# Performance work log

Measured on AMD Instinct MI355X. Metric: run time of the kernel, lower is better.

Reference implementation:

```python
import jax, jax.numpy as jnp
import numpy as np

N_NODES = 100000
N_EDGES = 1600000
NFEAT, NHID, NCLASS = 512, 128, 40


def setup_inputs() -> dict:
    key = jax.random.key(0)
    ks = jax.random.split(key, 8)
    x = jax.random.normal(ks[0], (N_NODES, NFEAT), dtype=jnp.float32)
    adj_row = jax.random.randint(ks[1], (N_EDGES,), 0, N_NODES, dtype=jnp.int64)
    adj_col = jax.random.randint(ks[2], (N_EDGES,), 0, N_NODES, dtype=jnp.int64)
    adj_val = jax.random.uniform(ks[3], (N_EDGES,), dtype=jnp.float32)
    W1 = jax.random.normal(ks[4], (NFEAT, NHID), dtype=jnp.float32) * (1.0 / np.sqrt(NHID))
    b1 = jax.random.normal(ks[5], (NHID,), dtype=jnp.float32) * 0.01
    W2 = jax.random.normal(ks[6], (NHID, NCLASS), dtype=jnp.float32) * (1.0 / np.sqrt(NCLASS))
    b2 = jax.random.normal(ks[7], (NCLASS,), dtype=jnp.float32) * 0.01
    return {"x": x, "adj_row": adj_row, "adj_col": adj_col, "adj_val": adj_val,
            "W1": W1, "b1": b1, "W2": W2, "b2": b2}


def _spmm(row, col, val, dense):
    # COO SpMM: out[r] = sum_e val[e] * dense[col[e]]  for edges with row[e]==r
    gathered = val[:, None] * dense[col]          # [E, F]
    return jax.ops.segment_sum(gathered, row, num_segments=N_NODES)


def reference(x, adj_row, adj_col, adj_val, W1, b1, W2, b2):
    # Layer 1: support = X @ W1; out = A @ support + b1; ReLU
    h = _spmm(adj_row, adj_col, adj_val, x @ W1) + b1
    h = jax.nn.relu(h)
    # dropout is identity in eval mode (training=False)
    # Layer 2
    logits = _spmm(adj_row, adj_col, adj_val, h @ W2) + b2
    return jax.nn.log_softmax(logits, axis=1)
```

## Files before the change

kernel.cpp:

```cpp
#include <hip/hip_runtime.h>
#include <hip/hip_bf16.h>
#include <math.h>

#define N_NODES 100000
#define N_EDGES 1600000
#define NFEAT 512
#define NHID 128
#define NCLASS 40
#define CAP 48
#define G1_ROWS 128
#define G1_BLOCKS ((N_NODES + G1_ROWS - 1) / G1_ROWS)
#define COUNT_BLOCKS ((N_EDGES + 1023) / 1024)
#define PITCH 520

typedef __attribute__((ext_vector_type(8))) short short8;
typedef __attribute__((ext_vector_type(4))) float floatx4;

__device__ __forceinline__ short f2bf(float f) {
    union { float f; unsigned u; } v; v.f = f;
    unsigned r = v.u + 0x7FFFu + ((v.u >> 16) & 1u);
    return (short)(r >> 16);
}
__device__ __forceinline__ float bf2f(unsigned short u) {
    union { unsigned u; float f; } v; v.u = ((unsigned)u) << 16;
    return v.f;
}
__device__ __forceinline__ unsigned pk2bf(float a, float b) {
    __hip_bfloat162 t = __float22bfloat162_rn(make_float2(a, b));
    union { __hip_bfloat162 h; unsigned u; } v; v.h = t;
    return v.u;
}

__global__ void convert_W1_kernel(const float* __restrict__ W1, unsigned short* __restrict__ W1T) {
    int i = blockIdx.x * 256 + threadIdx.x;
    int k = i >> 7, n = i & 127;
    W1T[(size_t)n * NFEAT + k] = (unsigned short)f2bf(W1[i]);
}

__global__ __launch_bounds__(512)
void gemm1_kernel(const float* __restrict__ x, const unsigned short* __restrict__ W1T,
                  unsigned short* __restrict__ out) {
    __shared__ unsigned short Bs[NHID * PITCH];
    int t = threadIdx.x;
    {
        const short8* src = (const short8*)W1T;
        #pragma unroll
        for (int i = 0; i < 16; i++) {
            int c = t + i * 512;
            int row = c >> 6;
            int col = (c & 63) * 8;
            *(short8*)&Bs[row * PITCH + col] = src[c];
        }
    }
    __syncthreads();

    int w = t >> 6, l = t & 63;
    int lane16 = l & 15, quad = l >> 4;
    int rowBase = blockIdx.x * G1_ROWS + w * 16;

    floatx4 acc[8];
    #pragma unroll
    for (int j = 0; j < 8; j++) acc[j] = (floatx4){0.f, 0.f, 0.f, 0.f};

    int gr = rowBase + lane16;
    if (gr >= N_NODES) gr = N_NODES - 1;
    const float* aRow = x + (size_t)gr * NFEAT + quad * 8;

    #pragma unroll 4
    for (int kc = 0; kc < NFEAT; kc += 32) {
        float4 v0 = *(const float4*)(aRow + kc);
        float4 v1 = *(const float4*)(aRow + kc + 4);
        union { short8 s; unsigned u[4]; } av;
        av.u[0] = pk2bf(v0.x, v0.y);
        av.u[1] = pk2bf(v0.z, v0.w);
        av.u[2] = pk2bf(v1.x, v1.y);
        av.u[3] = pk2bf(v1.z, v1.w);
        short8 afr = av.s;
        #pragma unroll
        for (int nt = 0; nt < 8; nt++) {
            short8 bfr = *(const short8*)&Bs[(nt * 16 + lane16) * PITCH + kc + quad * 8];
            acc[nt] = __builtin_amdgcn_mfma_f32_16x16x32_bf16(afr, bfr, acc[nt], 0, 0, 0);
        }
    }
    #pragma unroll
    for (int r = 0; r < 4; r++) {
        int gr2 = rowBase + quad * 4 + r;
        if (gr2 < N_NODES) {
            #pragma unroll
            for (int nt = 0; nt < 8; nt++)
                out[(size_t)gr2 * NHID + nt * 16 + lane16] =
                    (unsigned short)f2bf(acc[nt][r]);
        }
    }
}

__global__ __launch_bounds__(256)
void count_fill_kernel(const int* __restrict__ adj_row, const int* __restrict__ adj_col,
                       const float* __restrict__ adj_val,
                       int* __restrict__ counts, int2* __restrict__ csr) {
    int base = blockIdx.x * 1024 + threadIdx.x;
    #pragma unroll
    for (int i = 0; i < 4; i++) {
        int e = base + i * 256;
        if (e < N_EDGES) {
            int r = adj_row[e];
            int old = atomicAdd(&counts[r], 1);
            if (old < CAP)
                csr[(size_t)r * CAP + old] = make_int2(adj_col[e], __float_as_int(adj_val[e]));
        }
    }
}

__global__ __launch_bounds__(256)
void spmm1_kernel(const int* __restrict__ counts, const int2* __restrict__ csr,
                  const unsigned short* __restrict__ dense, const float* __restrict__ b1,
                  unsigned short* __restrict__ h) {
    int r = blockIdx.x * 4 + (threadIdx.x >> 6);
    int l = threadIdx.x & 63;
    int cnt = min(counts[r], CAP);
    int2 pk = (l < cnt) ? csr[(size_t)r * CAP + l] : make_int2(0, 0);
    float acc0 = 0.f, acc1 = 0.f;
    int j = 0;
    for (; j + 16 <= cnt; j += 16) {
        unsigned d[16];
        float v[16];
        #pragma unroll
        for (int q = 0; q < 16; q++) {
            int c = __shfl(pk.x, j + q);
            v[q] = __int_as_float(__shfl(pk.y, j + q));
            d[q] = *(const unsigned*)&dense[(size_t)c * NHID + l * 2];
        }
        #pragma unroll
        for (int q = 0; q < 16; q++) {
            acc0 += v[q] * bf2f((unsigned short)d[q]);
            acc1 += v[q] * bf2f((unsigned short)(d[q] >> 16));
        }
    }
    for (; j + 8 <= cnt; j += 8) {
        unsigned d[8];
        float v[8];
        #pragma unroll
        for (int q = 0; q < 8; q++) {
            int c = __shfl(pk.x, j + q);
            v[q] = __int_as_float(__shfl(pk.y, j + q));
            d[q] = *(const unsigned*)&dense[(size_t)c * NHID + l * 2];
        }
        #pragma unroll
        for (int q = 0; q < 8; q++) {
            acc0 += v[q] * bf2f((unsigned short)d[q]);
            acc1 += v[q] * bf2f((unsigned short)(d[q] >> 16));
        }
    }
    for (; j < cnt; j++) {
        int c = __shfl(pk.x, j);
        float v = __int_as_float(__shfl(pk.y, j));
        unsigned d = *(const unsigned*)&dense[(size_t)c * NHID + l * 2];
        acc0 += v * bf2f((unsigned short)d);
        acc1 += v * bf2f((unsigned short)(d >> 16));
    }
    float r0 = fmaxf(acc0 + b1[l * 2 + 0], 0.f);
    float r1 = fmaxf(acc1 + b1[l * 2 + 1], 0.f);
    *(unsigned*)&h[(size_t)r * NHID + l * 2] = pk2bf(r0, r1);
}

__global__ __launch_bounds__(256)
void gemm2_kernel(const unsigned short* __restrict__ h, const float* __restrict__ W2,
                  unsigned short* __restrict__ out) {
    __shared__ float W2s[NHID * NCLASS];
    __shared__ float hs[32][NHID];
    int t = threadIdx.x;
    for (int i = t; i < NHID * NCLASS; i += 256) W2s[i] = W2[i];
    int row0 = blockIdx.x * 32;
    {
        const unsigned* hsrc = (const unsigned*)(h + (size_t)row0 * NHID);
        #pragma unroll
        for (int j = 0; j < 8; j++) {
            int f = t * 8 + j;
            unsigned d = hsrc[f];
            hs[f >> 6][(f & 63) * 2 + 0] = bf2f((unsigned short)d);
            hs[f >> 6][(f & 63) * 2 + 1] = bf2f((unsigned short)(d >> 16));
        }
    }
    __syncthreads();
    int w = t >> 6, l = t & 63;
    if (l < NCLASS) {
        float acc[8];
        #pragma unroll
        for (int j = 0; j < 8; j++) acc[j] = 0.f;
        #pragma unroll 4
        for (int k = 0; k < NHID; k++) {
            float wk = W2s[k * NCLASS + l];
            #pragma unroll
            for (int j = 0; j < 8; j++) acc[j] += hs[w * 8 + j][k] * wk;
        }
        #pragma unroll
        for (int j = 0; j < 8; j++)
            out[(size_t)(row0 + w * 8 + j) * NCLASS + l] = (unsigned short)f2bf(acc[j]);
    }
}

__global__ __launch_bounds__(256)
void spmm2_kernel(const int* __restrict__ counts, const int2* __restrict__ csr,
                  const unsigned short* __restrict__ dense, const float* __restrict__ b2,
                  float* __restrict__ out) {
    int r = blockIdx.x * 4 + (threadIdx.x >> 6);
    int l = threadIdx.x & 63;
    int cnt = min(counts[r], CAP);
    int2 pk = (l < cnt) ? csr[(size_t)r * CAP + l] : make_int2(0, 0);
    float acc = 0.f;
    int j = 0;
    for (; j + 16 <= cnt; j += 16) {
        float v[16], f[16];
        #pragma unroll
        for (int q = 0; q < 16; q++) {
            int c = __shfl(pk.x, j + q);
            v[q] = __int_as_float(__shfl(pk.y, j + q));
            f[q] = (l < NCLASS) ? bf2f(dense[(size_t)c * NCLASS + l]) : 0.f;
        }
        #pragma unroll
        for (int q = 0; q < 16; q++) acc += v[q] * f[q];
    }
    for (; j + 8 <= cnt; j += 8) {
        float v[8], f[8];
        #pragma unroll
        for (int q = 0; q < 8; q++) {
            int c = __shfl(pk.x, j + q);
            v[q] = __int_as_float(__shfl(pk.y, j + q));
            f[q] = (l < NCLASS) ? bf2f(dense[(size_t)c * NCLASS + l]) : 0.f;
        }
        #pragma unroll
        for (int q = 0; q < 8; q++) acc += v[q] * f[q];
    }
    for (; j < cnt; j++) {
        int c = __shfl(pk.x, j);
        float v = __int_as_float(__shfl(pk.y, j));
        if (l < NCLASS) acc += v * bf2f(dense[(size_t)c * NCLASS + l]);
    }
    float logit = (l < NCLASS) ? (acc + b2[l]) : -INFINITY;
    float m = logit;
    #pragma unroll
    for (int o = 32; o >= 1; o >>= 1) m = fmaxf(m, __shfl_xor(m, o, 64));
    float e = (l < NCLASS) ? __expf(logit - m) : 0.f;
    float s = e;
    #pragma unroll
    for (int o = 32; o >= 1; o >>= 1) s += __shfl_xor(s, o, 64);
    if (l < NCLASS) out[(size_t)r * NCLASS + l] = logit - m - __logf(s);
}


extern "C" void kernel_launch(void* const* d_in, const int* in_sizes, int n_in,
                              void* d_out, int out_size, void* d_ws, size_t ws_size,
                              hipStream_t stream) {
    const float* x       = (const float*)d_in[0];
    const int*   adj_row = (const int*)d_in[1];
    const int*   adj_col = (const int*)d_in[2];
    const float* adj_val = (const float*)d_in[3];
    const float* W1      = (const float*)d_in[4];
    const float* b1      = (const float*)d_in[5];
    const float* W2      = (const float*)d_in[6];
    const float* b2      = (const float*)d_in[7];
    float* out = (float*)d_out;

    char* ws = (char*)d_ws;
    size_t off = 0;
    auto alloc = [&](size_t bytes) -> void* {
        void* p = ws + off;
        off += bytes;
        off = (off + 255) & ~(size_t)255;
        return p;
    };
    unsigned short* support1 = (unsigned short*)alloc((size_t)N_NODES * NHID * 2);
    unsigned short* h        = (unsigned short*)alloc((size_t)N_NODES * NHID * 2);
    unsigned short* W1T      = (unsigned short*)alloc((size_t)NFEAT * NHID * 2);
    int*   counts = (int*)alloc((size_t)N_NODES * 4);
    int2*  csr    = (int2*)alloc((size_t)N_NODES * CAP * 8);
    unsigned short* support2 = support1;

    hipMemsetAsync(counts, 0, (size_t)N_NODES * sizeof(int), stream);
    convert_W1_kernel<<<(NFEAT * NHID) / 256, 256, 0, stream>>>(W1, W1T);
    count_fill_kernel<<<COUNT_BLOCKS, 256, 0, stream>>>(adj_row, adj_col, adj_val,
                                                        counts, csr);
    gemm1_kernel<<<G1_BLOCKS, 512, 0, stream>>>(x, W1T, support1);
    spmm1_kernel<<<N_NODES / 4, 256, 0, stream>>>(counts, csr, support1, b1, h);
    gemm2_kernel<<<N_NODES / 32, 256, 0, stream>>>(h, W2, support2);
    spmm2_kernel<<<N_NODES / 4, 256, 0, stream>>>(counts, csr, support2, b2, out);
}
```

Before: 654.6 us.

## Replace global-atomic COO-to-ELL build with two-pass binned counting sort

Replaces the single count_fill kernel, which did one global atomicAdd per edge on the per-row counts, with a two-pass binned sort. Pass one builds per-block histograms over 256-row bins, scans them, and scatters packed edge records into bins using LDS atomics. Pass two fills the padded CSR per bin with LDS-local counters and writes the counts, so the memset is no longer needed. The aim is to cut global atomic contention and random scattered writes, at the cost of extra kernel launches, a serial single-block scan, and an extra pass through an intermediate buffer that reuses support1's storage.

Result: faster. 620.4 us (-5.2%).

```diff
diff --git a/kernel.cpp b/kernel.cpp
--- a/kernel.cpp
+++ b/kernel.cpp
@@ -10,8 +10,12 @@
 #define CAP 48
 #define G1_ROWS 128
 #define G1_BLOCKS ((N_NODES + G1_ROWS - 1) / G1_ROWS)
-#define COUNT_BLOCKS ((N_EDGES + 1023) / 1024)
 #define PITCH 520
+
+#define BIN_ROWS 256
+#define NBINS ((N_NODES + BIN_ROWS - 1) / BIN_ROWS)
+#define EPB 4096
+#define P1_BLOCKS ((N_EDGES + EPB - 1) / EPB)
 
 typedef __attribute__((ext_vector_type(8))) short short8;
 typedef __attribute__((ext_vector_type(4))) float floatx4;
@@ -35,6 +39,92 @@
     int i = blockIdx.x * 256 + threadIdx.x;
     int k = i >> 7, n = i & 127;
     W1T[(size_t)n * NFEAT + k] = (unsigned short)f2bf(W1[i]);
+}
+
+__global__ __launch_bounds__(256)
+void p1_hist_kernel(const int* __restrict__ adj_row, int* __restrict__ blockHist) {
+    __shared__ int hh[NBINS];
+    int t = threadIdx.x;
+    for (int i = t; i < NBINS; i += 256) hh[i] = 0;
+    __syncthreads();
+    int base = blockIdx.x * EPB;
+    #pragma unroll
+    for (int i = 0; i < EPB / 256; i++) {
+        int e = base + i * 256 + t;
+        if (e < N_EDGES) atomicAdd(&hh[adj_row[e] >> 8], 1);
+    }
+    __syncthreads();
+    for (int i = t; i < NBINS; i += 256)
+        blockHist[(size_t)blockIdx.x * NBINS + i] = hh[i];
+}
+
+__global__ __launch_bounds__(512)
+void p1_scan_kernel(int* __restrict__ blockHist) {
+    __shared__ int s[512];
+    int b = threadIdx.x;
+    int tot = 0;
+    if (b < NBINS)
+        for (int k = 0; k < P1_BLOCKS; k++) tot += blockHist[(size_t)k * NBINS + b];
+    s[b] = tot;
+    __syncthreads();
+    for (int ofs = 1; ofs < 512; ofs <<= 1) {
+        int w = (b >= ofs) ? s[b - ofs] : 0;
+        __syncthreads();
+        s[b] += w;
+        __syncthreads();
+    }
+    if (b < NBINS) {
+        int run = s[b] - tot;
+        for (int k = 0; k < P1_BLOCKS; k++) {
+            int tmp = blockHist[(size_t)k * NBINS + b];
+            blockHist[(size_t)k * NBINS + b] = run;
+            run += tmp;
+        }
+    }
+}
+
+__global__ __launch_bounds__(256)
+void p1_scatter_kernel(const int* __restrict__ adj_row, const int* __restrict__ adj_col,
+                       const float* __restrict__ adj_val,
+                       const int* __restrict__ blockHist, int2* __restrict__ recs) {
+    __shared__ int cur[NBINS];
+    int t = threadIdx.x;
+    for (int i = t; i < NBINS; i += 256)
+        cur[i] = blockHist[(size_t)blockIdx.x * NBINS + i];
+    __syncthreads();
+    int base = blockIdx.x * EPB;
+    #pragma unroll
+    for (int i = 0; i < EPB / 256; i++) {
+        int e = base + i * 256 + t;
+        if (e < N_EDGES) {
+            int r = adj_row[e];
+            int pos = atomicAdd(&cur[r >> 8], 1);
+            recs[pos] = make_int2(((r & 255) << 17) | adj_col[e],
+                                  __float_as_int(adj_val[e]));
+        }
+    }
+}
+
+__global__ __launch_bounds__(256)
+void p2_fill_kernel(const int2* __restrict__ recs, const int* __restrict__ blockHist,
+                    int* __restrict__ counts, int2* __restrict__ csr) {
+    __shared__ int cnt[BIN_ROWS];
+    int b = blockIdx.x, t = threadIdx.x;
+    cnt[t] = 0;
+    __syncthreads();
+    int beg = blockHist[b];
+    int end = (b + 1 < NBINS) ? blockHist[b + 1] : N_EDGES;
+    for (int i = beg + t; i < end; i += 256) {
+        int2 rec = recs[i];
+        int rl = ((unsigned)rec.x) >> 17;
+        int col = rec.x & 0x1FFFF;
+        int rank = atomicAdd(&cnt[rl], 1);
+        if (rank < CAP)
+            csr[(size_t)(b * BIN_ROWS + rl) * CAP + rank] = make_int2(col, rec.y);
+    }
+    __syncthreads();
+    int row = b * BIN_ROWS + t;
+    if (row < N_NODES) counts[row] = cnt[t];
 }
 
 __global__ __launch_bounds__(512)
@@ -90,23 +180,6 @@
             for (int nt = 0; nt < 8; nt++)
                 out[(size_t)gr2 * NHID + nt * 16 + lane16] =
                     (unsigned short)f2bf(acc[nt][r]);
-        }
-    }
-}
-
-__global__ __launch_bounds__(256)
-void count_fill_kernel(const int* __restrict__ adj_row, const int* __restrict__ adj_col,
-                       const float* __restrict__ adj_val,
-                       int* __restrict__ counts, int2* __restrict__ csr) {
-    int base = blockIdx.x * 1024 + threadIdx.x;
-    #pragma unroll
-    for (int i = 0; i < 4; i++) {
-        int e = base + i * 256;
-        if (e < N_EDGES) {
-            int r = adj_row[e];
-            int old = atomicAdd(&counts[r], 1);
-            if (old < CAP)
-                csr[(size_t)r * CAP + old] = make_int2(adj_col[e], __float_as_int(adj_val[e]));
         }
     }
 }
@@ -272,14 +345,18 @@
     unsigned short* support1 = (unsigned short*)alloc((size_t)N_NODES * NHID * 2);
     unsigned short* h        = (unsigned short*)alloc((size_t)N_NODES * NHID * 2);
     unsigned short* W1T      = (unsigned short*)alloc((size_t)NFEAT * NHID * 2);
-    int*   counts = (int*)alloc((size_t)N_NODES * 4);
-    int2*  csr    = (int2*)alloc((size_t)N_NODES * CAP * 8);
+    int*   counts    = (int*)alloc((size_t)N_NODES * 4);
+    int2*  csr       = (int2*)alloc((size_t)N_NODES * CAP * 8);
+    int*   blockHist = (int*)alloc((size_t)P1_BLOCKS * NBINS * 4);
+    int2*  recs      = (int2*)support1;
     unsigned short* support2 = support1;
 
-    hipMemsetAsync(counts, 0, (size_t)N_NODES * sizeof(int), stream);
     convert_W1_kernel<<<(NFEAT * NHID) / 256, 256, 0, stream>>>(W1, W1T);
-    count_fill_kernel<<<COUNT_BLOCKS, 256, 0, stream>>>(adj_row, adj_col, adj_val,
-                                                        counts, csr);
+    p1_hist_kernel<<<P1_BLOCKS, 256, 0, stream>>>(adj_row, blockHist);
+    p1_scan_kernel<<<1, 512, 0, stream>>>(blockHist);
+    p1_scatter_kernel<<<P1_BLOCKS, 256, 0, stream>>>(adj_row, adj_col, adj_val,
+                                                     blockHist, recs);
+    p2_fill_kernel<<<NBINS, 256, 0, stream>>>(recs, blockHist, counts, csr);
     gemm1_kernel<<<G1_BLOCKS, 512, 0, stream>>>(x, W1T, support1);
     spmm1_kernel<<<N_NODES / 4, 256, 0, stream>>>(counts, csr, support1, b1, h);
     gemm2_kernel<<<N_NODES / 32, 256, 0, stream>>>(h, W2, support2);
```
